# Kernel optimization log

Measured on AMD Instinct MI355X. Metric: run time of the kernel, lower is better.

## Reference

```python
import jax, jax.numpy as jnp
import numpy as np

N = 4096      # sentences in document
K = 32        # clusters (args.k)
D = 256       # input_dim
H = 128       # hidden_dim
P_SAL = 0.5   # args.percent_sal


def setup_inputs() -> dict:
    key = jax.random.key(0)
    ks = jax.random.split(key, 12)
    s = 1.0 / np.sqrt(H)
    inp = {
        "sent_gae_embeds": jax.random.normal(ks[0], (N, D), jnp.float32),
        "labels": jax.random.randint(ks[1], (N,), 0, K),
        # GRU layer 0 (torch gate order r,z,n)
        "W_ih0": jax.random.uniform(ks[2], (3 * H, D), jnp.float32, -s, s),
        "W_hh0": jax.random.uniform(ks[3], (3 * H, H), jnp.float32, -s, s),
        "b_ih0": jax.random.uniform(ks[4], (3 * H,), jnp.float32, -s, s),
        "b_hh0": jax.random.uniform(ks[5], (3 * H,), jnp.float32, -s, s),
        # GRU layer 1
        "W_ih1": jax.random.uniform(ks[6], (3 * H, H), jnp.float32, -s, s),
        "W_hh1": jax.random.uniform(ks[7], (3 * H, H), jnp.float32, -s, s),
        "b_ih1": jax.random.uniform(ks[8], (3 * H,), jnp.float32, -s, s),
        "b_hh1": jax.random.uniform(ks[9], (3 * H,), jnp.float32, -s, s),
        # weight-normed linear: W = g * v / ||v|| (norm over input dim)
        "lin_v": jax.random.normal(ks[10], (1, D + H), jnp.float32) * 0.05,
        "lin_g": jnp.ones((1, 1), jnp.float32),
        "lin_b": jnp.zeros((1,), jnp.float32),
    }
    return inp


def _gru_layer(x, W_ih, W_hh, b_ih, b_hh):
    # x: [T, B, Din] -> outputs [T, B, H]
    xw = jnp.einsum("tbd,gd->tbg", x, W_ih) + b_ih  # precompute input gates

    def step(h, xw_t):
        hw = h @ W_hh.T + b_hh
        r = jax.nn.sigmoid(xw_t[:, :H] + hw[:, :H])
        z = jax.nn.sigmoid(xw_t[:, H:2 * H] + hw[:, H:2 * H])
        n = jnp.tanh(xw_t[:, 2 * H:] + r * hw[:, 2 * H:])
        h_new = (1.0 - z) * n + z * h
        return h_new, h_new

    h0 = jnp.zeros((x.shape[1], H), x.dtype)
    _, outs = jax.lax.scan(step, h0, xw)
    return outs


def reference(sent_gae_embeds, labels, W_ih0, W_hh0, b_ih0, b_hh0,
              W_ih1, W_hh1, b_ih1, b_hh1, lin_v, lin_g, lin_b):
    # --- cluster gather: position of each sentence within its cluster ---
    onehot = jax.nn.one_hot(labels, K, dtype=jnp.int32)          # [N, K]
    pos = jnp.cumsum(onehot, axis=0)[jnp.arange(N), labels] - 1  # [N]
    lengths = onehot.sum(axis=0)                                 # [K]

    # padded per-cluster sequences: [T=N, B=K, D]
    padded = jnp.zeros((N, K, D), sent_gae_embeds.dtype).at[pos, labels].set(sent_gae_embeds)

    # --- 2-layer GRU over each cluster sequence ---
    h1 = _gru_layer(padded, W_ih0, W_hh0, b_ih0, b_hh0)
    h2 = _gru_layer(h1, W_ih1, W_hh1, b_ih1, b_hh1)
    len_c = jnp.maximum(lengths, 1)  # empty cluster -> length-1 zero sequence
    cluster_embeds = h2[len_c - 1, jnp.arange(K)]  # [K, H]

    # --- scatter cluster embeds back onto sentences (sent detached as in torch) ---
    sent_d = jax.lax.stop_gradient(sent_gae_embeds)
    final_embeds = jnp.concatenate([sent_d, cluster_embeds[labels]], axis=-1)  # [N, D+H]

    # weight-normed linear + tanh
    Wn = lin_g * lin_v / jnp.linalg.norm(lin_v, axis=1, keepdims=True)
    scores = jnp.tanh(final_embeds @ Wn.T + lin_b)[:, 0]  # [N]

    # salience: per-cluster segment-sum normalization
    clu_scores = jax.ops.segment_sum(scores, labels, num_segments=K)
    sal_scores = scores / clu_scores[labels]

    # position scores: max(0.5, exp(-(i+1)/n**(1/3)))
    inv = np.float32(1.0 / (N ** (1.0 / 3.0)))
    pos_scores = jnp.maximum(0.5, jnp.exp(-(jnp.arange(N, dtype=jnp.float32) + 1.0) * inv))

    return P_SAL * sal_scores + (1.0 - P_SAL) * pos_scores
```

## Files before the change

kernel.cpp:

```cpp
#include <hip/hip_runtime.h>
#include <cmath>

#define NN 4096
#define KK 32
#define DD 256
#define HH 128
#define G3 384
#define CH 16
#define RH 136

typedef __attribute__((ext_vector_type(8))) _Float16 h8;
typedef __attribute__((ext_vector_type(4))) float f32x4;

__global__ __launch_bounds__(256) void prep_k(
    const int* __restrict__ labels, const float* __restrict__ lin_v,
    const float* __restrict__ lin_g,
    const float* __restrict__ Whh0, const float* __restrict__ Wih1,
    const float* __restrict__ Whh1,
    const float* __restrict__ sent, const float* __restrict__ W_ih0,
    const float* __restrict__ b_ih0,
    int* __restrict__ order, int* __restrict__ len, float* __restrict__ scale,
    _Float16* __restrict__ P, float* __restrict__ xw) {
  const int blk = blockIdx.x;
  const int t = threadIdx.x;
  if (blk < 72) {
    const int gid = blk * 256 + t;
    const int lane = gid & 63;
    const int kt = (gid >> 6) & 3;
    const int nt = (gid >> 8) % 24;
    const int mat = (gid >> 8) / 24;
    const float* W = (mat == 0) ? Whh0 : (mat == 1 ? Wih1 : Whh1);
    const int n = nt * 16 + (lane & 15);
    const int kbase = kt * 32 + (lane >> 4) * 8;
    _Float16* dst = P + (size_t)gid * 8;
#pragma unroll
    for (int j = 0; j < 8; ++j) dst[j] = (_Float16)W[(size_t)n * HH + kbase + j];
    return;
  }
  if (blk < 80) {
    const int wv = t >> 6, lane = t & 63;
    const int c = (blk - 72) * 4 + wv;
    int count = 0;
    for (int base = 0; base < NN; base += 64) {
      const int i = base + lane;
      const bool f = (labels[i] == c);
      const unsigned long long m = __ballot(f);
      if (f) order[c * NN + count + __popcll(m & ((1ull << lane) - 1ull))] = i;
      count += __popcll(m);
    }
    if (lane == 0) len[c] = count;
    return;
  }
  if (blk == 80) {
    if (t < 64) {
      float s = 0.f;
      for (int j = t; j < G3; j += 64) { const float v = lin_v[j]; s += v * v; }
      for (int off = 32; off; off >>= 1) s += __shfl_down(s, off);
      if (t == 0) scale[0] = lin_g[0] / sqrtf(s);
    }
    return;
  }
  __shared__ float Xs[16][132];
  __shared__ float Ws[16][68];
  const int g = blk - 81;
  const int i0 = (g & 31) * 128;
  const int g0 = (g >> 5) * 64;
  const int it = t & 15;
  const int gt = t >> 4;
  float acc[8][4] = {};
  for (int k0 = 0; k0 < DD; k0 += 16) {
#pragma unroll
    for (int l = 0; l < 2; ++l) {
      const int u = t * 2 + l;
      const int r = u >> 2;
      const int cq = u & 3;
      const float4 f = *(const float4*)(sent + (size_t)(i0 + r) * DD + k0 + cq * 4);
      Xs[cq * 4 + 0][r] = f.x; Xs[cq * 4 + 1][r] = f.y;
      Xs[cq * 4 + 2][r] = f.z; Xs[cq * 4 + 3][r] = f.w;
    }
    {
      const int r = t >> 2;
      const int cq = t & 3;
      const float4 f = *(const float4*)(W_ih0 + (size_t)(g0 + r) * DD + k0 + cq * 4);
      Ws[cq * 4 + 0][r] = f.x; Ws[cq * 4 + 1][r] = f.y;
      Ws[cq * 4 + 2][r] = f.z; Ws[cq * 4 + 3][r] = f.w;
    }
    __syncthreads();
#pragma unroll
    for (int k = 0; k < 16; ++k) {
      float a[8], b[4];
#pragma unroll
      for (int x = 0; x < 8; ++x) a[x] = Xs[k][it * 8 + x];
#pragma unroll
      for (int y = 0; y < 4; ++y) b[y] = Ws[k][gt * 4 + y];
#pragma unroll
      for (int x = 0; x < 8; ++x)
#pragma unroll
        for (int y = 0; y < 4; ++y)
          acc[x][y] += a[x] * b[y];
    }
    __syncthreads();
  }
  const float4 bs = *(const float4*)(b_ih0 + g0 + gt * 4);
#pragma unroll
  for (int x = 0; x < 8; ++x) {
    const int gi = i0 + it * 8 + x;
    float4 o;
    o.x = acc[x][0] + bs.x; o.y = acc[x][1] + bs.y;
    o.z = acc[x][2] + bs.z; o.w = acc[x][3] + bs.w;
    *(float4*)(xw + (size_t)gi * G3 + g0 + gt * 4) = o;
  }
}

__global__ __launch_bounds__(768) void gru_fused_k(
    const float* __restrict__ xw0,
    const _Float16* __restrict__ pack,
    const float* __restrict__ b_hh0, const float* __restrict__ b_ih0,
    const float* __restrict__ b_ih1, const float* __restrict__ b_hh1,
    const int* __restrict__ len, const int* __restrict__ order,
    const float* __restrict__ sent,
    const float* __restrict__ lin_v, const float* __restrict__ scale,
    const float* __restrict__ lin_b, float* __restrict__ out) {
  const int c = blockIdx.x;
  const int t = threadIdx.x;
  const int wv = t >> 6, lane = t & 63;
  const int group = wv >> 2;
  const int v = wv & 3;
  h8 B[6][4];
  {
    const _Float16* mp = pack + (size_t)group * (24 * 4 * 64 * 8);
#pragma unroll
    for (int i = 0; i < 6; ++i) {
      const int nt = (i >> 1) * 8 + 2 * v + (i & 1);
#pragma unroll
      for (int kt = 0; kt < 4; ++kt)
        B[i][kt] = *(const h8*)(mp + ((size_t)(nt * 4 + kt) * 64 + lane) * 8);
    }
  }
  const int L = len[c];
  const int Lr = (L > 0) ? L : 1;
  const bool use_bih0 = (L == 0);
  const int u0 = t / 96, f0 = t - u0 * 96;
  const int u1 = (t + 768) / 96, f1 = (t + 768) - u1 * 96;
  __shared__ __align__(16) float xwbuf[2 * CH * G3];
  __shared__ __align__(16) _Float16 ring[16][2 * RH];
  __shared__ __align__(16) _Float16 hp2[2][2][HH];
  __shared__ float xw1buf[2][8][G3];
  __shared__ float ce_s[HH];
  __shared__ float vbuf[G3];
  __shared__ float sc_s[2048];
  __shared__ float sc_red;
  {
    _Float16* rp = &ring[0][0];
    for (int u = t; u < 16 * 2 * RH; u += 768) rp[u] = (_Float16)0.f;
  }
  if (t < HH) {
    hp2[0][0][t] = (_Float16)0.f; hp2[0][1][t] = (_Float16)0.f;
    hp2[1][0][t] = (_Float16)0.f; hp2[1][1][t] = (_Float16)0.f;
  }
  if (!use_bih0) {
    const float4* src = (const float4*)xw0;
    float4* dst = (float4*)xwbuf;
    const int r0 = (u0 < L) ? order[c * NN + u0] : 0;
    const int r1 = (u1 < L) ? order[c * NN + u1] : 0;
    dst[t] = src[(size_t)r0 * 96 + f0];
    dst[t + 768] = src[(size_t)r1 * 96 + f1];
  }
  const int tg = 32 * v + (lane & 31);
  float bhr = 0.f, bhz = 0.f, bhn = 0.f;
  float bir = 0.f, biz = 0.f, bin = 0.f;
  float h = 0.f;
  if (lane < 32) {
    if (group == 0) {
      bhr = b_hh0[tg]; bhz = b_hh0[HH + tg]; bhn = b_hh0[2 * HH + tg];
      if (use_bih0) {
        bir = b_ih0[tg]; biz = b_ih0[HH + tg]; bin = b_ih0[2 * HH + tg];
      }
    } else if (group == 2) {
      bhr = b_hh1[tg]; bhz = b_hh1[HH + tg]; bhn = b_hh1[2 * HH + tg];
      bir = b_ih1[tg]; biz = b_ih1[HH + tg]; bin = b_ih1[2 * HH + tg];
    }
  }
  __syncthreads();
  const int q = lane >> 4;
  const int row = lane & 15;
  const int hs = (row == 0 || row == 4) ? 0 : 1;
  const bool hiacc = ((lane >> 4) & 1) != 0;
  for (int it2 = 0; it2 < Lr + 9; ++it2) {
    const int par = it2 & 1;
    if (!use_bih0 && (it2 & (CH - 1)) == 0 && it2 + CH < Lr) {
      const float4* src = (const float4*)xw0;
      float4* dst = (float4*)(xwbuf + ((((it2 >> 4) + 1) & 1) ? CH * G3 : 0));
      const int p0 = it2 + CH + u0;
      const int p1 = it2 + CH + u1;
      const int r0 = (p0 < L) ? order[c * NN + p0] : 0;
      const int r1 = (p1 < L) ? order[c * NN + p1] : 0;
      dst[t] = src[(size_t)r0 * 96 + f0];
      dst[t + 768] = src[(size_t)r1 * 96 + f1];
    }
    if (group == 0) {
      if (it2 < Lr) {
        float xr = bir, xz = biz, xn = bin;
        if (!use_bih0 && lane < 32) {
          const float* xrow = xwbuf + ((it2 >> 4) & 1) * (CH * G3)
                                    + (it2 & (CH - 1)) * G3;
          xr = xrow[tg]; xz = xrow[HH + tg]; xn = xrow[2 * HH + tg];
        }
        const _Float16* abse = &ring[(it2 - 1) & 15][hs * RH];
        h8 A[4];
#pragma unroll
        for (int kt = 0; kt < 4; ++kt)
          A[kt] = *(const h8*)(abse + kt * 32 + q * 8);
        f32x4 a0[6];
#pragma unroll
        for (int i = 0; i < 6; ++i) {
          f32x4 a = {0.f, 0.f, 0.f, 0.f};
#pragma unroll
          for (int kt = 0; kt < 4; ++kt)
            a = __builtin_amdgcn_mfma_f32_16x16x32_f16(A[kt], B[i][kt], a, 0, 0, 0);
          a0[i] = a;
        }
        if (lane < 32) {
          const float hwrA = a0[0][0] + a0[0][1], hwrB = a0[1][0] + a0[1][1];
          const float hwzA = a0[2][0] + a0[2][1], hwzB = a0[3][0] + a0[3][1];
          const float hwnA = a0[4][0] + a0[4][1], hwnB = a0[5][0] + a0[5][1];
          const float hwr = hiacc ? hwrB : hwrA;
          const float hwz = hiacc ? hwzB : hwzA;
          const float hwn = hiacc ? hwnB : hwnA;
          const float r = 1.f / (1.f + __expf(-(xr + bhr + hwr)));
          const float z = 1.f / (1.f + __expf(-(xz + bhz + hwz)));
          float tgt = xn + r * (bhn + hwn);
          tgt = fminf(fmaxf(tgt, -15.f), 15.f);
          const float e = __expf(2.f * tgt);
          const float n = (e - 1.f) / (e + 1.f);
          h = (1.f - z) * n + z * h;
          const _Float16 hi = (_Float16)h;
          _Float16* rs = &ring[it2 & 15][0];
          rs[tg] = hi;  rs[RH + tg] = (_Float16)(h - (float)hi);
        }
      }
    } else if (group == 1) {
      if (it2 >= 8 && (it2 & 7) == 0 && it2 - 8 < Lr) {
        const int c8 = it2 - 8;
        const int m = lane & 15;
        const int s = m >> 1, half = m & 1;
        const _Float16* abse = &ring[(c8 + s) & 15][half * RH];
        h8 A[4];
#pragma unroll
        for (int kt = 0; kt < 4; ++kt)
          A[kt] = *(const h8*)(abse + kt * 32 + q * 8);
        const int cbuf = (c8 >> 3) & 1;
        float* xo0 = &xw1buf[cbuf][2 * q][0];
        float* xo1 = &xw1buf[cbuf][2 * q + 1][0];
#pragma unroll
        for (int i = 0; i < 6; ++i) {
          f32x4 a = {0.f, 0.f, 0.f, 0.f};
#pragma unroll
          for (int kt = 0; kt < 4; ++kt)
            a = __builtin_amdgcn_mfma_f32_16x16x32_f16(A[kt], B[i][kt], a, 0, 0, 0);
          const int nt = (i >> 1) * 8 + 2 * v + (i & 1);
          const int col = nt * 16 + (lane & 15);
          xo0[col] = a[0] + a[1];
          xo1[col] = a[2] + a[3];
        }
      }
    } else {
      if (it2 >= 9) {
        const int j = it2 - 9;
        float xr = 0.f, xz = 0.f, xn = 0.f;
        if (lane < 32) {
          const float* xi = xw1buf[(j >> 3) & 1][j & 7];
          xr = xi[tg] + bir; xz = xi[HH + tg] + biz; xn = xi[2 * HH + tg] + bin;
        }
        const _Float16* hbase = hp2[par][hs];
        h8 A[4];
#pragma unroll
        for (int kt = 0; kt < 4; ++kt)
          A[kt] = *(const h8*)(hbase + kt * 32 + q * 8);
        f32x4 a1[6];
#pragma unroll
        for (int i = 0; i < 6; ++i) {
          f32x4 a = {0.f, 0.f, 0.f, 0.f};
#pragma unroll
          for (int kt = 0; kt < 4; ++kt)
            a = __builtin_amdgcn_mfma_f32_16x16x32_f16(A[kt], B[i][kt], a, 0, 0, 0);
          a1[i] = a;
        }
        if (lane < 32) {
          const float hwrA = a1[0][0] + a1[0][1], hwrB = a1[1][0] + a1[1][1];
          const float hwzA = a1[2][0] + a1[2][1], hwzB = a1[3][0] + a1[3][1];
          const float hwnA = a1[4][0] + a1[4][1], hwnB = a1[5][0] + a1[5][1];
          const float hwr = hiacc ? hwrB : hwrA;
          const float hwz = hiacc ? hwzB : hwzA;
          const float hwn = hiacc ? hwnB : hwnA;
          const float r = 1.f / (1.f + __expf(-(xr + bhr + hwr)));
          const float z = 1.f / (1.f + __expf(-(xz + bhz + hwz)));
          float tgt = xn + r * (bhn + hwn);
          tgt = fminf(fmaxf(tgt, -15.f), 15.f);
          const float e = __expf(2.f * tgt);
          const float n = (e - 1.f) / (e + 1.f);
          h = (1.f - z) * n + z * h;
          const _Float16 hi = (_Float16)h;
          hp2[par ^ 1][0][tg] = hi;
          hp2[par ^ 1][1][tg] = (_Float16)(h - (float)hi);
        }
      }
    }
    __syncthreads();
  }
  if (L == 0) return;
  if (group == 2 && lane < 32) ce_s[tg] = h;
  if (t < G3) vbuf[t] = lin_v[t];
  __syncthreads();
  if (wv == 0) {
    float cd = ce_s[lane] * vbuf[DD + lane] + ce_s[64 + lane] * vbuf[DD + 64 + lane];
    for (int off = 32; off; off >>= 1) cd += __shfl_down(cd, off);
    if (lane == 0) sc_red = cd;
  }
  __syncthreads();
  const float cedot = sc_red;
  const float sc = scale[0], lb = lin_b[0];
  const int Lc = (L < 2048) ? L : 2048;
  for (int p = wv; p < Lc; p += 12) {
    const int i = order[c * NN + p];
    const float4 a = *(const float4*)(sent + (size_t)i * DD + lane * 4);
    const float4 b = ((const float4*)vbuf)[lane];
    float d = a.x * b.x + a.y * b.y + a.z * b.z + a.w * b.w;
    for (int off = 32; off; off >>= 1) d += __shfl_down(d, off);
    if (lane == 0) sc_s[p] = tanhf(sc * (d + cedot) + lb);
  }
  __syncthreads();
  if (wv == 0) {
    float s = 0.f;
    for (int p = lane; p < Lc; p += 64) s += sc_s[p];
    for (int off = 32; off; off >>= 1) s += __shfl_down(s, off);
    if (lane == 0) sc_red = 1.f / s;
  }
  __syncthreads();
  const float inv = sc_red;
  for (int p = t; p < Lc; p += 768) {
    const int i = order[c * NN + p];
    float ps = __expf(-(float)(i + 1) * 0.0625f);
    ps = fmaxf(0.5f, ps);
    out[i] = 0.5f * (sc_s[p] * inv) + 0.5f * ps;
  }
}

extern "C" void kernel_launch(void* const* d_in, const int* in_sizes, int n_in,
                              void* d_out, int out_size, void* d_ws, size_t ws_size,
                              hipStream_t stream) {
  const float* sent   = (const float*)d_in[0];
  const int*   labels = (const int*)d_in[1];
  const float* W_ih0  = (const float*)d_in[2];
  const float* W_hh0  = (const float*)d_in[3];
  const float* b_ih0  = (const float*)d_in[4];
  const float* b_hh0  = (const float*)d_in[5];
  const float* W_ih1  = (const float*)d_in[6];
  const float* W_hh1  = (const float*)d_in[7];
  const float* b_ih1  = (const float*)d_in[8];
  const float* b_hh1  = (const float*)d_in[9];
  const float* lin_v  = (const float*)d_in[10];
  const float* lin_g  = (const float*)d_in[11];
  const float* lin_b  = (const float*)d_in[12];
  float* out = (float*)d_out;

  char* ws = (char*)d_ws;
  size_t off = 0;
  auto alloc = [&](size_t bytes) -> void* {
    void* p = ws + off;
    off = (off + bytes + 255) & ~(size_t)255;
    return p;
  };
  int*   order  = (int*)  alloc((size_t)KK * NN * sizeof(int));
  int*   len    = (int*)  alloc(KK * sizeof(int));
  float* scale  = (float*)alloc(sizeof(float));
  _Float16* pack = (_Float16*)alloc((size_t)18432 * 8 * sizeof(_Float16));
  float* xw     = (float*)alloc((size_t)NN * G3 * sizeof(float));
  (void)ws_size; (void)in_sizes; (void)n_in; (void)out_size;

  prep_k<<<dim3(273), dim3(256), 0, stream>>>(
      labels, lin_v, lin_g, W_hh0, W_ih1, W_hh1,
      sent, W_ih0, b_ih0, order, len, scale, pack, xw);
  gru_fused_k<<<dim3(KK), dim3(768), 0, stream>>>(
      xw, pack, b_hh0, b_ih0, b_ih1, b_hh1, len, order,
      sent, lin_v, scale, lin_b, out);
}
```

Measured before the change: 241.2 us.

## Fuse prep kernel into single GRU kernel with in-block MFMA input projection

```diff
diff --git a/kernel.cpp b/kernel.cpp
--- a/kernel.cpp
+++ b/kernel.cpp
@@ -12,144 +12,32 @@
 typedef __attribute__((ext_vector_type(8))) _Float16 h8;
 typedef __attribute__((ext_vector_type(4))) float f32x4;
 
-__global__ __launch_bounds__(256) void prep_k(
-    const int* __restrict__ labels, const float* __restrict__ lin_v,
-    const float* __restrict__ lin_g,
-    const float* __restrict__ Whh0, const float* __restrict__ Wih1,
-    const float* __restrict__ Whh1,
-    const float* __restrict__ sent, const float* __restrict__ W_ih0,
-    const float* __restrict__ b_ih0,
-    int* __restrict__ order, int* __restrict__ len, float* __restrict__ scale,
-    _Float16* __restrict__ P, float* __restrict__ xw) {
-  const int blk = blockIdx.x;
-  const int t = threadIdx.x;
-  if (blk < 72) {
-    const int gid = blk * 256 + t;
-    const int lane = gid & 63;
-    const int kt = (gid >> 6) & 3;
-    const int nt = (gid >> 8) % 24;
-    const int mat = (gid >> 8) / 24;
-    const float* W = (mat == 0) ? Whh0 : (mat == 1 ? Wih1 : Whh1);
-    const int n = nt * 16 + (lane & 15);
-    const int kbase = kt * 32 + (lane >> 4) * 8;
-    _Float16* dst = P + (size_t)gid * 8;
-#pragma unroll
-    for (int j = 0; j < 8; ++j) dst[j] = (_Float16)W[(size_t)n * HH + kbase + j];
-    return;
-  }
-  if (blk < 80) {
-    const int wv = t >> 6, lane = t & 63;
-    const int c = (blk - 72) * 4 + wv;
-    int count = 0;
-    for (int base = 0; base < NN; base += 64) {
-      const int i = base + lane;
-      const bool f = (labels[i] == c);
-      const unsigned long long m = __ballot(f);
-      if (f) order[c * NN + count + __popcll(m & ((1ull << lane) - 1ull))] = i;
-      count += __popcll(m);
-    }
-    if (lane == 0) len[c] = count;
-    return;
-  }
-  if (blk == 80) {
-    if (t < 64) {
-      float s = 0.f;
-      for (int j = t; j < G3; j += 64) { const float v = lin_v[j]; s += v * v; }
-      for (int off = 32; off; off >>= 1) s += __shfl_down(s, off);
-      if (t == 0) scale[0] = lin_g[0] / sqrtf(s);
-    }
-    return;
-  }
-  __shared__ float Xs[16][132];
-  __shared__ float Ws[16][68];
-  const int g = blk - 81;
-  const int i0 = (g & 31) * 128;
-  const int g0 = (g >> 5) * 64;
-  const int it = t & 15;
-  const int gt = t >> 4;
-  float acc[8][4] = {};
-  for (int k0 = 0; k0 < DD; k0 += 16) {
-#pragma unroll
-    for (int l = 0; l < 2; ++l) {
-      const int u = t * 2 + l;
-      const int r = u >> 2;
-      const int cq = u & 3;
-      const float4 f = *(const float4*)(sent + (size_t)(i0 + r) * DD + k0 + cq * 4);
-      Xs[cq * 4 + 0][r] = f.x; Xs[cq * 4 + 1][r] = f.y;
-      Xs[cq * 4 + 2][r] = f.z; Xs[cq * 4 + 3][r] = f.w;
-    }
-    {
-      const int r = t >> 2;
-      const int cq = t & 3;
-      const float4 f = *(const float4*)(W_ih0 + (size_t)(g0 + r) * DD + k0 + cq * 4);
-      Ws[cq * 4 + 0][r] = f.x; Ws[cq * 4 + 1][r] = f.y;
-      Ws[cq * 4 + 2][r] = f.z; Ws[cq * 4 + 3][r] = f.w;
-    }
-    __syncthreads();
-#pragma unroll
-    for (int k = 0; k < 16; ++k) {
-      float a[8], b[4];
-#pragma unroll
-      for (int x = 0; x < 8; ++x) a[x] = Xs[k][it * 8 + x];
-#pragma unroll
-      for (int y = 0; y < 4; ++y) b[y] = Ws[k][gt * 4 + y];
-#pragma unroll
-      for (int x = 0; x < 8; ++x)
-#pragma unroll
-        for (int y = 0; y < 4; ++y)
-          acc[x][y] += a[x] * b[y];
-    }
-    __syncthreads();
-  }
-  const float4 bs = *(const float4*)(b_ih0 + g0 + gt * 4);
-#pragma unroll
-  for (int x = 0; x < 8; ++x) {
-    const int gi = i0 + it * 8 + x;
-    float4 o;
-    o.x = acc[x][0] + bs.x; o.y = acc[x][1] + bs.y;
-    o.z = acc[x][2] + bs.z; o.w = acc[x][3] + bs.w;
-    *(float4*)(xw + (size_t)gi * G3 + g0 + gt * 4) = o;
-  }
-}
-
-__global__ __launch_bounds__(768) void gru_fused_k(
-    const float* __restrict__ xw0,
-    const _Float16* __restrict__ pack,
-    const float* __restrict__ b_hh0, const float* __restrict__ b_ih0,
+__global__ __launch_bounds__(768) void gru_one_k(
+    const float* __restrict__ sent, const int* __restrict__ labels,
+    const float* __restrict__ W_ih0, const float* __restrict__ W_hh0,
+    const float* __restrict__ b_ih0, const float* __restrict__ b_hh0,
+    const float* __restrict__ W_ih1, const float* __restrict__ W_hh1,
     const float* __restrict__ b_ih1, const float* __restrict__ b_hh1,
-    const int* __restrict__ len, const int* __restrict__ order,
-    const float* __restrict__ sent,
-    const float* __restrict__ lin_v, const float* __restrict__ scale,
+    const float* __restrict__ lin_v, const float* __restrict__ lin_g,
     const float* __restrict__ lin_b, float* __restrict__ out) {
   const int c = blockIdx.x;
   const int t = threadIdx.x;
   const int wv = t >> 6, lane = t & 63;
   const int group = wv >> 2;
   const int v = wv & 3;
-  h8 B[6][4];
-  {
-    const _Float16* mp = pack + (size_t)group * (24 * 4 * 64 * 8);
-#pragma unroll
-    for (int i = 0; i < 6; ++i) {
-      const int nt = (i >> 1) * 8 + 2 * v + (i & 1);
-#pragma unroll
-      for (int kt = 0; kt < 4; ++kt)
-        B[i][kt] = *(const h8*)(mp + ((size_t)(nt * 4 + kt) * 64 + lane) * 8);
-    }
-  }
-  const int L = len[c];
-  const int Lr = (L > 0) ? L : 1;
-  const bool use_bih0 = (L == 0);
-  const int u0 = t / 96, f0 = t - u0 * 96;
-  const int u1 = (t + 768) / 96, f1 = (t + 768) - u1 * 96;
+  const int q = lane >> 4;
+
   __shared__ __align__(16) float xwbuf[2 * CH * G3];
   __shared__ __align__(16) _Float16 ring[16][2 * RH];
   __shared__ __align__(16) _Float16 hp2[2][2][HH];
   __shared__ float xw1buf[2][8][G3];
+  __shared__ int order_s[NN];
+  __shared__ int cnt_s[12];
   __shared__ float ce_s[HH];
   __shared__ float vbuf[G3];
   __shared__ float sc_s[2048];
-  __shared__ float sc_red;
+  __shared__ float sc_red, sc_scale;
+
   {
     _Float16* rp = &ring[0][0];
     for (int u = t; u < 16 * 2 * RH; u += 768) rp[u] = (_Float16)0.f;
@@ -158,13 +46,66 @@
     hp2[0][0][t] = (_Float16)0.f; hp2[0][1][t] = (_Float16)0.f;
     hp2[1][0][t] = (_Float16)0.f; hp2[1][1][t] = (_Float16)0.f;
   }
-  if (!use_bih0) {
-    const float4* src = (const float4*)xw0;
-    float4* dst = (float4*)xwbuf;
-    const int r0 = (u0 < L) ? order[c * NN + u0] : 0;
-    const int r1 = (u1 < L) ? order[c * NN + u1] : 0;
-    dst[t] = src[(size_t)r0 * 96 + f0];
-    dst[t + 768] = src[(size_t)r1 * 96 + f1];
+  const int ch0 = (wv * 64) / 12;
+  const int ch1 = ((wv + 1) * 64) / 12;
+  {
+    int cnt = 0;
+    for (int ch = ch0; ch < ch1; ++ch) {
+      const unsigned long long m = __ballot(labels[ch * 64 + lane] == c);
+      cnt += __popcll(m);
+    }
+    if (lane == 0) cnt_s[wv] = cnt;
+  }
+  __syncthreads();
+  int off = 0, Ltot = 0;
+#pragma unroll
+  for (int j = 0; j < 12; ++j) {
+    const int cj = cnt_s[j];
+    if (j < wv) off += cj;
+    Ltot += cj;
+  }
+  for (int ch = ch0; ch < ch1; ++ch) {
+    const int i = ch * 64 + lane;
+    const bool f = (labels[i] == c);
+    const unsigned long long m = __ballot(f);
+    if (f) order_s[off + __popcll(m & ((1ull << lane) - 1ull))] = i;
+    off += __popcll(m);
+  }
+  const int L = Ltot;
+  const int Lr = (L > 0) ? L : 1;
+  const bool use_bih0 = (L == 0);
+
+  h8 B[6][4];
+  {
+    const float* Wm = (group == 0) ? W_hh0 : (group == 1 ? W_ih1 : W_hh1);
+#pragma unroll
+    for (int i = 0; i < 6; ++i) {
+      const int nt = (i >> 1) * 8 + 2 * v + (i & 1);
+      const int n = nt * 16 + (lane & 15);
+#pragma unroll
+      for (int kt = 0; kt < 4; ++kt) {
+        const float* wp = Wm + (size_t)n * HH + kt * 32 + q * 8;
+        const float4 fa = *(const float4*)(wp);
+        const float4 fb = *(const float4*)(wp + 4);
+        B[i][kt] = (h8){(_Float16)fa.x, (_Float16)fa.y, (_Float16)fa.z,
+                        (_Float16)fa.w, (_Float16)fb.x, (_Float16)fb.y,
+                        (_Float16)fb.z, (_Float16)fb.w};
+      }
+    }
+  }
+  h8 BI[2][8];
+#pragma unroll
+  for (int ii = 0; ii < 2; ++ii) {
+    const int n = (2 * wv + ii) * 16 + (lane & 15);
+#pragma unroll
+    for (int kt = 0; kt < 8; ++kt) {
+      const float* wp = W_ih0 + (size_t)n * DD + kt * 32 + q * 8;
+      const float4 fa = *(const float4*)(wp);
+      const float4 fb = *(const float4*)(wp + 4);
+      BI[ii][kt] = (h8){(_Float16)fa.x, (_Float16)fa.y, (_Float16)fa.z,
+                        (_Float16)fa.w, (_Float16)fb.x, (_Float16)fb.y,
+                        (_Float16)fb.z, (_Float16)fb.w};
+    }
   }
   const int tg = 32 * v + (lane & 31);
   float bhr = 0.f, bhz = 0.f, bhn = 0.f;
@@ -173,38 +114,57 @@
   if (lane < 32) {
     if (group == 0) {
       bhr = b_hh0[tg]; bhz = b_hh0[HH + tg]; bhn = b_hh0[2 * HH + tg];
-      if (use_bih0) {
-        bir = b_ih0[tg]; biz = b_ih0[HH + tg]; bin = b_ih0[2 * HH + tg];
-      }
+      bir = b_ih0[tg]; biz = b_ih0[HH + tg]; bin = b_ih0[2 * HH + tg];
     } else if (group == 2) {
       bhr = b_hh1[tg]; bhz = b_hh1[HH + tg]; bhn = b_hh1[2 * HH + tg];
       bir = b_ih1[tg]; biz = b_ih1[HH + tg]; bin = b_ih1[2 * HH + tg];
     }
   }
   __syncthreads();
-  const int q = lane >> 4;
+
+  auto compute_chunk = [&](int base, int half) {
+    const int p = base + (lane & 15);
+    const int rowi = (p < L) ? order_s[p] : 0;
+    const float* sp = sent + (size_t)rowi * DD + q * 8;
+    h8 AI[8];
+#pragma unroll
+    for (int kt = 0; kt < 8; ++kt) {
+      const float4 fa = *(const float4*)(sp + kt * 32);
+      const float4 fb = *(const float4*)(sp + kt * 32 + 4);
+      AI[kt] = (h8){(_Float16)fa.x, (_Float16)fa.y, (_Float16)fa.z,
+                    (_Float16)fa.w, (_Float16)fb.x, (_Float16)fb.y,
+                    (_Float16)fb.z, (_Float16)fb.w};
+    }
+    float* dstb = xwbuf + half * (CH * G3);
+#pragma unroll
+    for (int ii = 0; ii < 2; ++ii) {
+      f32x4 a = {0.f, 0.f, 0.f, 0.f};
+#pragma unroll
+      for (int kt = 0; kt < 8; ++kt)
+        a = __builtin_amdgcn_mfma_f32_16x16x32_f16(AI[kt], BI[ii][kt], a, 0, 0, 0);
+      const int col = (2 * wv + ii) * 16 + (lane & 15);
+#pragma unroll
+      for (int reg = 0; reg < 4; ++reg)
+        dstb[(q * 4 + reg) * G3 + col] = a[reg];
+    }
+  };
+  if (!use_bih0) compute_chunk(0, 0);
+  __syncthreads();
+
   const int row = lane & 15;
   const int hs = (row == 0 || row == 4) ? 0 : 1;
   const bool hiacc = ((lane >> 4) & 1) != 0;
   for (int it2 = 0; it2 < Lr + 9; ++it2) {
     const int par = it2 & 1;
-    if (!use_bih0 && (it2 & (CH - 1)) == 0 && it2 + CH < Lr) {
-      const float4* src = (const float4*)xw0;
-      float4* dst = (float4*)(xwbuf + ((((it2 >> 4) + 1) & 1) ? CH * G3 : 0));
-      const int p0 = it2 + CH + u0;
-      const int p1 = it2 + CH + u1;
-      const int r0 = (p0 < L) ? order[c * NN + p0] : 0;
-      const int r1 = (p1 < L) ? order[c * NN + p1] : 0;
-      dst[t] = src[(size_t)r0 * 96 + f0];
-      dst[t + 768] = src[(size_t)r1 * 96 + f1];
-    }
+    if (!use_bih0 && (it2 & (CH - 1)) == 0 && it2 + CH < Lr)
+      compute_chunk(it2 + CH, ((it2 >> 4) + 1) & 1);
     if (group == 0) {
       if (it2 < Lr) {
         float xr = bir, xz = biz, xn = bin;
         if (!use_bih0 && lane < 32) {
           const float* xrow = xwbuf + ((it2 >> 4) & 1) * (CH * G3)
                                     + (it2 & (CH - 1)) * G3;
-          xr = xrow[tg]; xz = xrow[HH + tg]; xn = xrow[2 * HH + tg];
+          xr += xrow[tg]; xz += xrow[HH + tg]; xn += xrow[2 * HH + tg];
         }
         const _Float16* abse = &ring[(it2 - 1) & 15][hs * RH];
         h8 A[4];
@@ -314,32 +274,41 @@
   __syncthreads();
   if (wv == 0) {
     float cd = ce_s[lane] * vbuf[DD + lane] + ce_s[64 + lane] * vbuf[DD + 64 + lane];
-    for (int off = 32; off; off >>= 1) cd += __shfl_down(cd, off);
-    if (lane == 0) sc_red = cd;
+    float s2 = 0.f;
+#pragma unroll
+    for (int j = 0; j < 6; ++j) {
+      const float vv = vbuf[j * 64 + lane];
+      s2 += vv * vv;
+    }
+    for (int o = 32; o; o >>= 1) {
+      cd += __shfl_down(cd, o);
+      s2 += __shfl_down(s2, o);
+    }
+    if (lane == 0) { sc_red = cd; sc_scale = lin_g[0] / sqrtf(s2); }
   }
   __syncthreads();
   const float cedot = sc_red;
-  const float sc = scale[0], lb = lin_b[0];
+  const float sc = sc_scale, lb = lin_b[0];
   const int Lc = (L < 2048) ? L : 2048;
   for (int p = wv; p < Lc; p += 12) {
-    const int i = order[c * NN + p];
+    const int i = order_s[p];
     const float4 a = *(const float4*)(sent + (size_t)i * DD + lane * 4);
     const float4 b = ((const float4*)vbuf)[lane];
     float d = a.x * b.x + a.y * b.y + a.z * b.z + a.w * b.w;
-    for (int off = 32; off; off >>= 1) d += __shfl_down(d, off);
+    for (int o = 32; o; o >>= 1) d += __shfl_down(d, o);
     if (lane == 0) sc_s[p] = tanhf(sc * (d + cedot) + lb);
   }
   __syncthreads();
   if (wv == 0) {
     float s = 0.f;
     for (int p = lane; p < Lc; p += 64) s += sc_s[p];
-    for (int off = 32; off; off >>= 1) s += __shfl_down(s, off);
+    for (int o = 32; o; o >>= 1) s += __shfl_down(s, o);
     if (lane == 0) sc_red = 1.f / s;
   }
   __syncthreads();
   const float inv = sc_red;
   for (int p = t; p < Lc; p += 768) {
-    const int i = order[c * NN + p];
+    const int i = order_s[p];
     float ps = __expf(-(float)(i + 1) * 0.0625f);
     ps = fmaxf(0.5f, ps);
     out[i] = 0.5f * (sc_s[p] * inv) + 0.5f * ps;
@@ -363,25 +332,9 @@
   const float* lin_g  = (const float*)d_in[11];
   const float* lin_b  = (const float*)d_in[12];
   float* out = (float*)d_out;
-
-  char* ws = (char*)d_ws;
-  size_t off = 0;
-  auto alloc = [&](size_t bytes) -> void* {
-    void* p = ws + off;
-    off = (off + bytes + 255) & ~(size_t)255;
-    return p;
-  };
-  int*   order  = (int*)  alloc((size_t)KK * NN * sizeof(int));
-  int*   len    = (int*)  alloc(KK * sizeof(int));
-  float* scale  = (float*)alloc(sizeof(float));
-  _Float16* pack = (_Float16*)alloc((size_t)18432 * 8 * sizeof(_Float16));
-  float* xw     = (float*)alloc((size_t)NN * G3 * sizeof(float));
-  (void)ws_size; (void)in_sizes; (void)n_in; (void)out_size;
-
-  prep_k<<<dim3(273), dim3(256), 0, stream>>>(
-      labels, lin_v, lin_g, W_hh0, W_ih1, W_hh1,
-      sent, W_ih0, b_ih0, order, len, scale, pack, xw);
-  gru_fused_k<<<dim3(KK), dim3(768), 0, stream>>>(
-      xw, pack, b_hh0, b_ih0, b_ih1, b_hh1, len, order,
-      sent, lin_v, scale, lin_b, out);
+  (void)d_ws; (void)ws_size; (void)in_sizes; (void)n_in; (void)out_size;
+
+  gru_one_k<<<dim3(KK), dim3(768), 0, stream>>>(
+      sent, labels, W_ih0, W_hh0, b_ih0, b_hh0,
+      W_ih1, W_hh1, b_ih1, b_hh1, lin_v, lin_g, lin_b, out);
 }
```

Result: slower. 411.8 us (+70.7%).
